# Kernel tuning notes

Measured on AMD Instinct MI355X. Metric: run time of the kernel, lower is better.

Reference implementation:

```python
import jax, jax.numpy as jnp
import numpy as np

NEG_SLOPE = 0.2  # leaky_relu negative slope (alpha)

def _glorot(key, shape):
    fan_in, fan_out = shape[0], shape[-1]
    lim = jnp.sqrt(6.0 / (fan_in + fan_out))
    return jax.random.uniform(key, shape, jnp.float32, -lim, lim)

def setup_inputs() -> dict:
    key = jax.random.key(0)
    ks = jax.random.split(key, 10)
    N, E, F_IN, HID, HEADS, NCLASS = 50000, 800000, 512, 32, 8, 32
    x = jax.random.normal(ks[0], (N, F_IN), jnp.float32)
    edge_index = jax.random.randint(ks[1], (2, E), 0, N, jnp.int64)
    # layer 1: heads=8, out per head = 32, concat -> 256
    W1 = _glorot(ks[2], (F_IN, HEADS * HID))
    att_src1 = _glorot(ks[3], (HEADS, HID))
    att_dst1 = _glorot(ks[4], (HEADS, HID))
    b1 = jnp.zeros((HEADS * HID,), jnp.float32)
    # layer 2: heads=1, out = nclass
    W2 = _glorot(ks[5], (HEADS * HID, NCLASS))
    att_src2 = _glorot(ks[6], (1, NCLASS))
    att_dst2 = _glorot(ks[7], (1, NCLASS))
    b2 = jnp.zeros((NCLASS,), jnp.float32)
    return {"x": x, "edge_index": edge_index, "W1": W1, "att_src1": att_src1,
            "att_dst1": att_dst1, "b1": b1, "W2": W2, "att_src2": att_src2,
            "att_dst2": att_dst2, "b2": b2}

def gat_conv(x, src, dst, W, a_src, a_dst, bias, num_nodes):
    """PyG GATConv (eval mode, self loops already appended to src/dst)."""
    H, C = a_src.shape
    h = (x @ W).reshape(num_nodes, H, C)                 # [N,H,C]
    score_src = jnp.einsum('nhc,hc->nh', h, a_src)       # [N,H]
    score_dst = jnp.einsum('nhc,hc->nh', h, a_dst)       # [N,H]
    e = jax.nn.leaky_relu(score_src[src] + score_dst[dst], NEG_SLOPE)  # [E,H]
    m = jax.ops.segment_max(e, dst, num_segments=num_nodes)           # [N,H]
    w = jnp.exp(e - m[dst])
    denom = jax.ops.segment_sum(w, dst, num_segments=num_nodes)       # [N,H]
    alpha = w / (denom[dst] + 1e-16)                                  # [E,H]
    out = jax.ops.segment_sum(alpha[:, :, None] * h[src], dst,
                              num_segments=num_nodes)                 # [N,H,C]
    return out.reshape(num_nodes, H * C) + bias

def reference(x, edge_index, W1, att_src1, att_dst1, b1, W2, att_src2, att_dst2, b2):
    N = x.shape[0]
    loops = jnp.arange(N, dtype=edge_index.dtype)
    src = jnp.concatenate([edge_index[0], loops])  # PyG add_self_loops=True
    dst = jnp.concatenate([edge_index[1], loops])
    h = jax.nn.elu(gat_conv(x, src, dst, W1, att_src1, att_dst1, b1, N))
    out = gat_conv(h, src, dst, W2, att_src2, att_dst2, b2, N)
    return out + 1e-06
```

## Files before the change

### kernel.cpp

```cpp
#include <hip/hip_runtime.h>
#include <math.h>

#define N_NODES 50000
#define N_EDGES 800000
#define E2 (N_EDGES + N_NODES)
#define F_IN 512
#define HEADS 8
#define HID 32
#define HC 256
#define NCLASS 32
#define NEG_SLOPE 0.2f
#define ELLW 64

typedef unsigned int uint;
typedef unsigned short ushort;
typedef __attribute__((ext_vector_type(8))) short bf16x8;
typedef __attribute__((ext_vector_type(4))) float f32x4;

#define GLOBAL_LOAD_LDS16(g, l) \
    __builtin_amdgcn_global_load_lds((const __attribute__((address_space(1))) void*)(g), \
                                     (__attribute__((address_space(3))) void*)(l), 16, 0, 0)

__device__ inline uint bf16_rne_bits(float f) {
    uint u = __float_as_uint(f);
    return (u + 0x7fffu + ((u >> 16) & 1u)) >> 16;
}
__device__ inline float bf2f(ushort u) { return __uint_as_float(((uint)u) << 16); }

#define W1_BLOCKS 512
#define W2_BLOCKS 32

__global__ void __launch_bounds__(256) prep_kernel(const float* __restrict__ W1,
        ushort* __restrict__ w1hi, const float* __restrict__ W2, ushort* __restrict__ w2hi) {
    int b = blockIdx.x;
    if (b < W1_BLOCKS) {
        int t = b * 256 + threadIdx.x;
        int n = t >> 9, k = t & 511;
        w1hi[t] = (ushort)bf16_rne_bits(W1[k * 256 + n]);
    } else {
        int t = (b - W1_BLOCKS) * 256 + threadIdx.x;
        int n = t >> 8, k = t & 255;
        w2hi[t] = (ushort)bf16_rne_bits(W2[k * 32 + n]);
    }
}

#define NWG1 (((N_NODES + 127) / 128) * 2)
#define FILL_BLOCKS ((E2 / 4 + 255) / 256)

__global__ void __launch_bounds__(256) gemm1_mfma_kernel(const uint* __restrict__ xp,
        const ushort* __restrict__ bhi,
        const float* __restrict__ as1, const float* __restrict__ ad1,
        ushort* __restrict__ C, float* __restrict__ ssrc, float* __restrict__ sdst, int M,
        const int* __restrict__ ei, int* __restrict__ cursor, int* __restrict__ ell) {
    __shared__ uint   As[128 * 32];
    __shared__ ushort Bh[128 * 32];

    if (blockIdx.x >= NWG1) {
        int e0 = ((blockIdx.x - NWG1) * 256 + threadIdx.x) * 4;
        if (e0 < E2) {
            int src[4], dst[4];
            if (e0 < N_EDGES) {
                int4 s4 = *(const int4*)(ei + e0);
                int4 d4 = *(const int4*)(ei + N_EDGES + e0);
                src[0] = s4.x; src[1] = s4.y; src[2] = s4.z; src[3] = s4.w;
                dst[0] = d4.x; dst[1] = d4.y; dst[2] = d4.z; dst[3] = d4.w;
            } else {
                #pragma unroll
                for (int j = 0; j < 4; ++j) { src[j] = e0 + j - N_EDGES; dst[j] = src[j]; }
            }
            #pragma unroll
            for (int j = 0; j < 4; ++j) {
                int d = dst[j];
                int p = atomicAdd(&cursor[d], 1);
                ell[d * ELLW + p] = src[j];
            }
        }
        return;
    }

    const int tid = threadIdx.x, lane = tid & 63, wave = tid >> 6;

    const int orig = blockIdx.x;
    const int xcd = orig & 7, idx = orig >> 3;
    const int q = NWG1 >> 3, r = NWG1 & 7;
    const int nid = (xcd < r ? xcd * (q + 1) : r * (q + 1) + (xcd - r) * q) + idx;
    const int bm = (nid >> 1) * 128, bn = (nid & 1) * 128;

    const uint* agp[4]; const uint* alp[4];
    #pragma unroll
    for (int s = 0; s < 4; ++s) {
        int t = wave * 4 + s;
        int p = t * 64 + lane;
        int row = p >> 3, cs = p & 7;
        int c = cs ^ (row & 7);
        int grow = bm + row; if (grow > M - 1) grow = M - 1;
        agp[s] = xp + ((size_t)grow * 512 + c * 4);
        alp[s] = &As[t * 256];
    }
    const ushort* bhgp[2]; const ushort* bhlp[2];
    #pragma unroll
    for (int s = 0; s < 2; ++s) {
        int t = wave * 2 + s;
        int p = t * 64 + lane;
        int row = p >> 2, qs = p & 3;
        int qq = qs ^ ((row >> 1) & 3);
        size_t go = (size_t)(bn + row) * 512 + qq * 8;
        bhgp[s] = bhi + go;
        bhlp[s] = &Bh[t * 512];
    }

    f32x4 acc[4][4] = {};
    const int wm = (wave >> 1) * 64, wn = (wave & 1) * 64;
    const int fm = lane & 15, quad = lane >> 4;

    for (int kk = 0; kk < 16; ++kk) {
        #pragma unroll
        for (int s = 0; s < 4; ++s) GLOBAL_LOAD_LDS16(agp[s], alp[s]);
        #pragma unroll
        for (int s = 0; s < 2; ++s) GLOBAL_LOAD_LDS16(bhgp[s], bhlp[s]);
        #pragma unroll
        for (int s = 0; s < 4; ++s) agp[s] += 32;
        #pragma unroll
        for (int s = 0; s < 2; ++s) bhgp[s] += 32;
        __syncthreads();

        bf16x8 ah[4], al[4], bh[4];
        #pragma unroll
        for (int i = 0; i < 4; ++i) {
            int row = wm + i * 16 + fm;
            int sw = row & 7;
            uint4 c0 = *(const uint4*)&As[row * 32 + (((2 * quad)     ^ sw) * 4)];
            uint4 c1 = *(const uint4*)&As[row * 32 + (((2 * quad + 1) ^ sw) * 4)];
            union { uint u[4]; bf16x8 v; } H, L;
            H.u[0] = __builtin_amdgcn_perm(c0.y, c0.x, 0x07060302u);
            H.u[1] = __builtin_amdgcn_perm(c0.w, c0.z, 0x07060302u);
            H.u[2] = __builtin_amdgcn_perm(c1.y, c1.x, 0x07060302u);
            H.u[3] = __builtin_amdgcn_perm(c1.w, c1.z, 0x07060302u);
            uint r0 = __float_as_uint(__uint_as_float(c0.x) - __uint_as_float(c0.x & 0xffff0000u));
            uint r1 = __float_as_uint(__uint_as_float(c0.y) - __uint_as_float(c0.y & 0xffff0000u));
            uint r2 = __float_as_uint(__uint_as_float(c0.z) - __uint_as_float(c0.z & 0xffff0000u));
            uint r3 = __float_as_uint(__uint_as_float(c0.w) - __uint_as_float(c0.w & 0xffff0000u));
            uint r4 = __float_as_uint(__uint_as_float(c1.x) - __uint_as_float(c1.x & 0xffff0000u));
            uint r5 = __float_as_uint(__uint_as_float(c1.y) - __uint_as_float(c1.y & 0xffff0000u));
            uint r6 = __float_as_uint(__uint_as_float(c1.z) - __uint_as_float(c1.z & 0xffff0000u));
            uint r7 = __float_as_uint(__uint_as_float(c1.w) - __uint_as_float(c1.w & 0xffff0000u));
            L.u[0] = __builtin_amdgcn_perm(r1, r0, 0x07060302u);
            L.u[1] = __builtin_amdgcn_perm(r3, r2, 0x07060302u);
            L.u[2] = __builtin_amdgcn_perm(r5, r4, 0x07060302u);
            L.u[3] = __builtin_amdgcn_perm(r7, r6, 0x07060302u);
            ah[i] = H.v; al[i] = L.v;
        }
        #pragma unroll
        for (int j = 0; j < 4; ++j) {
            int row = wn + j * 16 + fm;
            int qs = quad ^ ((row >> 1) & 3);
            bh[j] = *(const bf16x8*)&Bh[row * 32 + qs * 8];
        }
        #pragma unroll
        for (int i = 0; i < 4; ++i)
            #pragma unroll
            for (int j = 0; j < 4; ++j) {
                acc[i][j] = __builtin_amdgcn_mfma_f32_16x16x32_bf16(ah[i], bh[j], acc[i][j], 0, 0, 0);
                acc[i][j] = __builtin_amdgcn_mfma_f32_16x16x32_bf16(al[i], bh[j], acc[i][j], 0, 0, 0);
            }
        __syncthreads();
    }

    #pragma unroll
    for (int i = 0; i < 4; ++i) {
        int rb = bm + wm + i * 16 + quad * 4;
        #pragma unroll
        for (int j = 0; j < 4; ++j) {
            int col = bn + wn + j * 16 + fm;
            #pragma unroll
            for (int r2_ = 0; r2_ < 4; ++r2_) {
                int row = rb + r2_;
                if (row < M) C[(size_t)row * 256 + col] = (ushort)bf16_rne_bits(acc[i][j][r2_]);
            }
        }
    }

    const int head0 = (bn + wn) >> 5;
    const float asA0 = as1[head0 * 32 + fm],      asA1 = as1[head0 * 32 + 16 + fm];
    const float asB0 = as1[head0 * 32 + 32 + fm], asB1 = as1[head0 * 32 + 48 + fm];
    const float adA0 = ad1[head0 * 32 + fm],      adA1 = ad1[head0 * 32 + 16 + fm];
    const float adB0 = ad1[head0 * 32 + 32 + fm], adB1 = ad1[head0 * 32 + 48 + fm];
    #pragma unroll
    for (int i = 0; i < 4; ++i) {
        #pragma unroll
        for (int r2_ = 0; r2_ < 4; ++r2_) {
            int row = bm + wm + i * 16 + quad * 4 + r2_;
            float s1A = acc[i][0][r2_] * asA0 + acc[i][1][r2_] * asA1;
            float s1B = acc[i][2][r2_] * asB0 + acc[i][3][r2_] * asB1;
            float s2A = acc[i][0][r2_] * adA0 + acc[i][1][r2_] * adA1;
            float s2B = acc[i][2][r2_] * adB0 + acc[i][3][r2_] * adB1;
            #pragma unroll
            for (int off = 1; off < 16; off <<= 1) {
                s1A += __shfl_xor(s1A, off);
                s1B += __shfl_xor(s1B, off);
                s2A += __shfl_xor(s2A, off);
                s2B += __shfl_xor(s2B, off);
            }
            if (fm == 0 && row < M) {
                ssrc[(size_t)row * 8 + head0]     = s1A;
                ssrc[(size_t)row * 8 + head0 + 1] = s1B;
                sdst[(size_t)row * 8 + head0]     = s2A;
                sdst[(size_t)row * 8 + head0 + 1] = s2B;
            }
        }
    }
}

__global__ void __launch_bounds__(256) gemm2_mfma_kernel(const ushort* __restrict__ A,
        const ushort* __restrict__ bh_g,
        const float* __restrict__ as2, const float* __restrict__ ad2,
        ushort* __restrict__ C, float* __restrict__ ssrc, float* __restrict__ sdst, int M) {
    const int tid = threadIdx.x, lane = tid & 63, wave = tid >> 6;
    const int bm = blockIdx.x * 128;
    const int fm = lane & 15, quad = lane >> 4;
    const int wrow = wave * 32;

    int gr[2];
    #pragma unroll
    for (int i = 0; i < 2; ++i) {
        gr[i] = bm + wrow + i * 16 + fm;
        if (gr[i] > M - 1) gr[i] = M - 1;
    }

    f32x4 acc[2][2] = {};
    for (int kk = 0; kk < 8; ++kk) {
        bf16x8 a[2], bh[2];
        #pragma unroll
        for (int i = 0; i < 2; ++i)
            a[i] = *(const bf16x8*)(A + (size_t)gr[i] * 256 + kk * 32 + quad * 8);
        #pragma unroll
        for (int j = 0; j < 2; ++j) {
            size_t off = (size_t)(j * 16 + fm) * 256 + kk * 32 + quad * 8;
            bh[j] = *(const bf16x8*)(bh_g + off);
        }
        #pragma unroll
        for (int i = 0; i < 2; ++i)
            #pragma unroll
            for (int j = 0; j < 2; ++j)
                acc[i][j] = __builtin_amdgcn_mfma_f32_16x16x32_bf16(a[i], bh[j], acc[i][j], 0, 0, 0);
    }

    float a0 = as2[fm], a1 = as2[16 + fm];
    float d0 = ad2[fm], d1 = ad2[16 + fm];
    #pragma unroll
    for (int i = 0; i < 2; ++i) {
        #pragma unroll
        for (int r2_ = 0; r2_ < 4; ++r2_) {
            int rg = bm + wrow + i * 16 + quad * 4 + r2_;
            float v0 = acc[i][0][r2_], v1 = acc[i][1][r2_];
            float s1 = v0 * a0 + v1 * a1;
            float s2 = v0 * d0 + v1 * d1;
            #pragma unroll
            for (int off = 1; off < 16; off <<= 1) {
                s1 += __shfl_xor(s1, off);
                s2 += __shfl_xor(s2, off);
            }
            if (rg < M) {
                C[(size_t)rg * 32 + fm]      = (ushort)bf16_rne_bits(v0);
                C[(size_t)rg * 32 + 16 + fm] = (ushort)bf16_rne_bits(v1);
                if (fm == 0) { ssrc[rg] = s1; sdst[rg] = s2; }
            }
        }
    }
}

__global__ void __launch_bounds__(256) agg1_wave_kernel(const ushort* __restrict__ h,
        const float* __restrict__ ssrc, const float* __restrict__ sdst,
        const int* __restrict__ cnt, const int* __restrict__ ell,
        const float* __restrict__ bias, ushort* __restrict__ out) {
    const int wid = (blockIdx.x * blockDim.x + threadIdx.x) >> 6;
    if (wid >= N_NODES) return;
    const int lane = threadIdx.x & 63;
    const int hg = lane >> 3;
    const int hl = lane & 7;
    const int n = wid;
    const int beg = n * ELLW;
    const int end = beg + cnt[n];
    const float sdst_n = sdst[(size_t)n * HEADS + hg];

    float4 acc = make_float4(0.f, 0.f, 0.f, 0.f);
    float sw = 0.f;
    const ushort* hc = h + lane * 4;
    const int base = hg << 3;
    for (int e = beg; e < end; e += 16) {
        int ee0 = e + hl, ee1 = e + 8 + hl;
        int ei0 = ee0 < end ? ee0 : end - 1;
        int ei1 = ee1 < end ? ee1 : end - 1;
        int s0 = ell[ei0];
        int s1 = ell[ei1];
        float c0 = ssrc[(size_t)s0 * HEADS + hg] + sdst_n;
        float c1 = ssrc[(size_t)s1 * HEADS + hg] + sdst_n;
        c0 = c0 > 0.f ? c0 : NEG_SLOPE * c0;
        c1 = c1 > 0.f ? c1 : NEG_SLOPE * c1;
        float w0 = (ee0 < end) ? __expf(c0) : 0.f;
        float w1 = (ee1 < end) ? __expf(c1) : 0.f;
        float wj[16]; int sj[16];
        #pragma unroll
        for (int j = 0; j < 8; ++j) {
            wj[j]     = __shfl(w0, base + j);
            sj[j]     = __shfl(s0, base + j);
            wj[8 + j] = __shfl(w1, base + j);
            sj[8 + j] = __shfl(s1, base + j);
        }
        ushort4 v[16];
        #pragma unroll
        for (int j = 0; j < 16; ++j) v[j] = *(const ushort4*)(hc + (size_t)sj[j] * HC);
        #pragma unroll
        for (int j = 0; j < 16; ++j) {
            acc.x += wj[j] * bf2f(v[j].x);
            acc.y += wj[j] * bf2f(v[j].y);
            acc.z += wj[j] * bf2f(v[j].z);
            acc.w += wj[j] * bf2f(v[j].w);
            sw += wj[j];
        }
    }
    float inv = 1.f / (sw + 1e-16f);
    float4 bv = *(const float4*)(bias + lane * 4);
    float4 o;
    o.x = acc.x * inv + bv.x; o.y = acc.y * inv + bv.y;
    o.z = acc.z * inv + bv.z; o.w = acc.w * inv + bv.w;
    o.x = o.x > 0.f ? o.x : expm1f(o.x);
    o.y = o.y > 0.f ? o.y : expm1f(o.y);
    o.z = o.z > 0.f ? o.z : expm1f(o.z);
    o.w = o.w > 0.f ? o.w : expm1f(o.w);
    ushort4 ob;
    ob.x = (ushort)bf16_rne_bits(o.x);
    ob.y = (ushort)bf16_rne_bits(o.y);
    ob.z = (ushort)bf16_rne_bits(o.z);
    ob.w = (ushort)bf16_rne_bits(o.w);
    *(ushort4*)(out + (size_t)n * HC + lane * 4) = ob;
}

__global__ void __launch_bounds__(256) agg2_kernel(const ushort* __restrict__ h2,
        const float* __restrict__ ssrc, const float* __restrict__ sdst,
        const int* __restrict__ cnt, const int* __restrict__ ell,
        const float* __restrict__ bias, float* __restrict__ out) {
    const int n = blockIdx.x * 4 + (threadIdx.x >> 6);
    if (n >= N_NODES) return;
    const int beg = n * ELLW;
    const int end = beg + cnt[n];
    const int t = threadIdx.x & 63;
    const float sdst_n = sdst[n];

    const int slot = t >> 4, cp = t & 15;
    float a0 = 0.f, a1 = 0.f, sw = 0.f;
    for (int e = beg + slot; e < end; e += 4) {
        int src = ell[e];
        float sc = ssrc[src] + sdst_n;
        sc = sc > 0.f ? sc : NEG_SLOPE * sc;
        float w = __expf(sc);
        uint v = *(const uint*)(h2 + (size_t)src * NCLASS + cp * 2);
        a0 += w * __uint_as_float(v << 16);
        a1 += w * __uint_as_float(v & 0xffff0000u);
        sw += w;
    }
    a0 += __shfl_down(a0, 32); a1 += __shfl_down(a1, 32); sw += __shfl_down(sw, 32);
    a0 += __shfl_down(a0, 16); a1 += __shfl_down(a1, 16); sw += __shfl_down(sw, 16);
    if (t < 16) {
        float inv = 1.f / (sw + 1e-16f);
        float2 o;
        o.x = a0 * inv + bias[cp * 2]     + 1e-6f;
        o.y = a1 * inv + bias[cp * 2 + 1] + 1e-6f;
        *(float2*)(out + (size_t)n * NCLASS + cp * 2) = o;
    }
}

extern "C" void kernel_launch(void* const* d_in, const int* in_sizes, int n_in,
                              void* d_out, int out_size, void* d_ws, size_t ws_size,
                              hipStream_t stream) {
    const float* x        = (const float*)d_in[0];
    const int*   ei       = (const int*)  d_in[1];
    const float* W1       = (const float*)d_in[2];
    const float* att_src1 = (const float*)d_in[3];
    const float* att_dst1 = (const float*)d_in[4];
    const float* b1       = (const float*)d_in[5];
    const float* W2       = (const float*)d_in[6];
    const float* att_src2 = (const float*)d_in[7];
    const float* att_dst2 = (const float*)d_in[8];
    const float* b2       = (const float*)d_in[9];
    float* out = (float*)d_out;

    ushort* w1t_hi = (ushort*)d_ws;
    ushort* w2t_hi = w1t_hi + 256 * 512;
    ushort* h1b    = w2t_hi + 32 * 256;
    ushort* h2b    = h1b + (size_t)N_NODES * HC;
    ushort* out1b  = h2b + (size_t)N_NODES * NCLASS;
    float* ssrc1 = (float*)(out1b + (size_t)N_NODES * HC);
    float* sdst1 = ssrc1 + (size_t)N_NODES * HEADS;
    float* ssrc2 = sdst1 + (size_t)N_NODES * HEADS;
    float* sdst2 = ssrc2 + N_NODES;
    int* cursor  = (int*)(sdst2 + N_NODES);
    int* ell     = cursor + N_NODES;

    hipMemsetAsync(cursor, 0, N_NODES * sizeof(int), stream);
    prep_kernel<<<W1_BLOCKS + W2_BLOCKS, 256, 0, stream>>>(W1, w1t_hi, W2, w2t_hi);

    gemm1_mfma_kernel<<<NWG1 + FILL_BLOCKS, 256, 0, stream>>>((const uint*)x, w1t_hi,
            att_src1, att_dst1, h1b, ssrc1, sdst1, N_NODES, ei, cursor, ell);
    agg1_wave_kernel<<<(N_NODES + 3) / 4, 256, 0, stream>>>(h1b, ssrc1, sdst1, cursor, ell, b1, out1b);

    gemm2_mfma_kernel<<<(N_NODES + 127) / 128, 256, 0, stream>>>(out1b, w2t_hi,
            att_src2, att_dst2, h2b, ssrc2, sdst2, N_NODES);
    agg2_kernel<<<(N_NODES + 3) / 4, 256, 0, stream>>>(h2b, ssrc2, sdst2, cursor, ell, b2, out);
}
```

Measured before the change: 328.3 us.

## Fuse layer-2 projection and attention scores into layer-1 aggregation kernel

Removes the separate gemm2 MFMA kernel and the bf16 intermediate out1b buffer. Each aggregation block stages W2 (16 KB) in shared memory, and each wave computes the 32-wide projection of its node with scalar FMAs and 32 full-wave shuffle reductions. Lane 0 then writes h2 and the layer-2 src/dst scores. This saves a kernel launch and a write and re-read of the N×256 activation. In exchange it adds a W2 load per block, many shuffles per node, and CUDA-core math in place of MFMA. The projection now uses the fp32 ELU output instead of a bf16-rounded copy.

Measured after the change: 397.6 us. 1.21x slower.

```diff
diff --git a/kernel.cpp b/kernel.cpp
--- a/kernel.cpp
+++ b/kernel.cpp
@@ -211,68 +211,21 @@
     }
 }
 
-__global__ void __launch_bounds__(256) gemm2_mfma_kernel(const ushort* __restrict__ A,
-        const ushort* __restrict__ bh_g,
-        const float* __restrict__ as2, const float* __restrict__ ad2,
-        ushort* __restrict__ C, float* __restrict__ ssrc, float* __restrict__ sdst, int M) {
-    const int tid = threadIdx.x, lane = tid & 63, wave = tid >> 6;
-    const int bm = blockIdx.x * 128;
-    const int fm = lane & 15, quad = lane >> 4;
-    const int wrow = wave * 32;
-
-    int gr[2];
-    #pragma unroll
-    for (int i = 0; i < 2; ++i) {
-        gr[i] = bm + wrow + i * 16 + fm;
-        if (gr[i] > M - 1) gr[i] = M - 1;
-    }
-
-    f32x4 acc[2][2] = {};
-    for (int kk = 0; kk < 8; ++kk) {
-        bf16x8 a[2], bh[2];
-        #pragma unroll
-        for (int i = 0; i < 2; ++i)
-            a[i] = *(const bf16x8*)(A + (size_t)gr[i] * 256 + kk * 32 + quad * 8);
-        #pragma unroll
-        for (int j = 0; j < 2; ++j) {
-            size_t off = (size_t)(j * 16 + fm) * 256 + kk * 32 + quad * 8;
-            bh[j] = *(const bf16x8*)(bh_g + off);
-        }
-        #pragma unroll
-        for (int i = 0; i < 2; ++i)
-            #pragma unroll
-            for (int j = 0; j < 2; ++j)
-                acc[i][j] = __builtin_amdgcn_mfma_f32_16x16x32_bf16(a[i], bh[j], acc[i][j], 0, 0, 0);
-    }
-
-    float a0 = as2[fm], a1 = as2[16 + fm];
-    float d0 = ad2[fm], d1 = ad2[16 + fm];
-    #pragma unroll
-    for (int i = 0; i < 2; ++i) {
-        #pragma unroll
-        for (int r2_ = 0; r2_ < 4; ++r2_) {
-            int rg = bm + wrow + i * 16 + quad * 4 + r2_;
-            float v0 = acc[i][0][r2_], v1 = acc[i][1][r2_];
-            float s1 = v0 * a0 + v1 * a1;
-            float s2 = v0 * d0 + v1 * d1;
-            #pragma unroll
-            for (int off = 1; off < 16; off <<= 1) {
-                s1 += __shfl_xor(s1, off);
-                s2 += __shfl_xor(s2, off);
-            }
-            if (rg < M) {
-                C[(size_t)rg * 32 + fm]      = (ushort)bf16_rne_bits(v0);
-                C[(size_t)rg * 32 + 16 + fm] = (ushort)bf16_rne_bits(v1);
-                if (fm == 0) { ssrc[rg] = s1; sdst[rg] = s2; }
-            }
-        }
-    }
-}
-
-__global__ void __launch_bounds__(256) agg1_wave_kernel(const ushort* __restrict__ h,
+__global__ void __launch_bounds__(256) agg1_fused_kernel(const ushort* __restrict__ h,
         const float* __restrict__ ssrc, const float* __restrict__ sdst,
         const int* __restrict__ cnt, const int* __restrict__ ell,
-        const float* __restrict__ bias, ushort* __restrict__ out) {
+        const float* __restrict__ bias, const ushort* __restrict__ w2hi,
+        const float* __restrict__ as2, const float* __restrict__ ad2,
+        ushort* __restrict__ h2b, float* __restrict__ ssrc2, float* __restrict__ sdst2) {
+    __shared__ ushort W2s[32 * 256];
+    {
+        const uint4* src = (const uint4*)w2hi;
+        uint4* dst = (uint4*)W2s;
+        #pragma unroll
+        for (int i = 0; i < 4; ++i) dst[threadIdx.x + i * 256] = src[threadIdx.x + i * 256];
+    }
+    __syncthreads();
+
     const int wid = (blockIdx.x * blockDim.x + threadIdx.x) >> 6;
     if (wid >= N_NODES) return;
     const int lane = threadIdx.x & 63;
@@ -328,12 +281,32 @@
     o.y = o.y > 0.f ? o.y : expm1f(o.y);
     o.z = o.z > 0.f ? o.z : expm1f(o.z);
     o.w = o.w > 0.f ? o.w : expm1f(o.w);
-    ushort4 ob;
-    ob.x = (ushort)bf16_rne_bits(o.x);
-    ob.y = (ushort)bf16_rne_bits(o.y);
-    ob.z = (ushort)bf16_rne_bits(o.z);
-    ob.w = (ushort)bf16_rne_bits(o.w);
-    *(ushort4*)(out + (size_t)n * HC + lane * 4) = ob;
+
+    float p[32];
+    #pragma unroll
+    for (int c = 0; c < 32; ++c) {
+        ushort4 w = *(const ushort4*)&W2s[c * 256 + lane * 4];
+        p[c] = o.x * bf2f(w.x) + o.y * bf2f(w.y) + o.z * bf2f(w.z) + o.w * bf2f(w.w);
+    }
+    #pragma unroll
+    for (int c = 0; c < 32; ++c)
+        #pragma unroll
+        for (int off = 1; off < 64; off <<= 1)
+            p[c] += __shfl_xor(p[c], off);
+    if (lane == 0) {
+        float s1 = 0.f, s2 = 0.f;
+        #pragma unroll
+        for (int c = 0; c < 32; ++c) {
+            s1 += p[c] * as2[c];
+            s2 += p[c] * ad2[c];
+        }
+        #pragma unroll
+        for (int c = 0; c < 32; c += 2) {
+            uint lo = bf16_rne_bits(p[c]), hi = bf16_rne_bits(p[c + 1]);
+            *(uint*)&h2b[(size_t)n * 32 + c] = lo | (hi << 16);
+        }
+        ssrc2[n] = s1; sdst2[n] = s2;
+    }
 }
 
 __global__ void __launch_bounds__(256) agg2_kernel(const ushort* __restrict__ h2,
@@ -389,8 +362,7 @@
     ushort* w2t_hi = w1t_hi + 256 * 512;
     ushort* h1b    = w2t_hi + 32 * 256;
     ushort* h2b    = h1b + (size_t)N_NODES * HC;
-    ushort* out1b  = h2b + (size_t)N_NODES * NCLASS;
-    float* ssrc1 = (float*)(out1b + (size_t)N_NODES * HC);
+    float* ssrc1 = (float*)(h2b + (size_t)N_NODES * NCLASS);
     float* sdst1 = ssrc1 + (size_t)N_NODES * HEADS;
     float* ssrc2 = sdst1 + (size_t)N_NODES * HEADS;
     float* sdst2 = ssrc2 + N_NODES;
@@ -402,9 +374,9 @@
 
     gemm1_mfma_kernel<<<NWG1 + FILL_BLOCKS, 256, 0, stream>>>((const uint*)x, w1t_hi,
             att_src1, att_dst1, h1b, ssrc1, sdst1, N_NODES, ei, cursor, ell);
-    agg1_wave_kernel<<<(N_NODES + 3) / 4, 256, 0, stream>>>(h1b, ssrc1, sdst1, cursor, ell, b1, out1b);
-
-    gemm2_mfma_kernel<<<(N_NODES + 127) / 128, 256, 0, stream>>>(out1b, w2t_hi,
-            att_src2, att_dst2, h2b, ssrc2, sdst2, N_NODES);
+
+    agg1_fused_kernel<<<(N_NODES + 3) / 4, 256, 0, stream>>>(h1b, ssrc1, sdst1, cursor, ell,
+            b1, w2t_hi, att_src2, att_dst2, h2b, ssrc2, sdst2);
+
     agg2_kernel<<<(N_NODES + 3) / 4, 256, 0, stream>>>(h2b, ssrc2, sdst2, cursor, ell, b2, out);
 }
```
